# Performance work log

Hardware: AMD Instinct MI355X
Metric: run time of the kernel (lower is better)

## Reference

```python
import math
import jax
import jax.numpy as jnp
import numpy as np

N = 65536      # n_particles(4) * batch(16384)
Z = 2          # z_dim
CTX = 128      # ctx_dim
H = 128        # drift_hidden
TE = 32        # time_emb_dim
T = 51         # n_integration_steps + 1
MAX_FREQ = 10.0


def setup_inputs() -> dict:
    key = jax.random.key(0)
    ks = jax.random.split(key, 18)
    rn = lambda k, shp, s=1.0: (jax.random.normal(k, shp, dtype=jnp.float32) * s)
    d_in = Z + CTX + TE   # 162, drift MLP input
    c_in = Z + CTX + 1    # 131, cnf field MLP input
    return {
        'z0': rn(ks[0], (N, Z)),
        'posterior_ctx': rn(ks[1], (N, CTX)),
        'cnf_ctx': rn(ks[2], (N, CTX)),
        'times': jnp.linspace(0.0, 1.0, T, dtype=jnp.float32),
        'xi': rn(ks[3], (T - 1, N, Z)),  # pre-drawn Euler-Maruyama noise
        'freqs': jnp.exp(jnp.linspace(0.0, math.log(MAX_FREQ), TE // 2)).astype(jnp.float32),
        'log_diff': jnp.float32(-3.0),
        'W1': rn(ks[4], (d_in, H), 1.0 / math.sqrt(d_in)),
        'b1': jnp.zeros((H,), jnp.float32),
        'W2': rn(ks[5], (H, H), 1.0 / math.sqrt(H)),
        'b2': jnp.zeros((H,), jnp.float32),
        'W3': rn(ks[6], (H, Z), 1.0 / math.sqrt(H)),
        'b3': jnp.zeros((Z,), jnp.float32),
        'V1': rn(ks[7], (c_in, H), 1.0 / math.sqrt(c_in)),
        'c1': jnp.zeros((H,), jnp.float32),
        'V2': rn(ks[8], (H, H), 1.0 / math.sqrt(H)),
        'c2': jnp.zeros((H,), jnp.float32),
        'V3': rn(ks[9], (H, Z), 1.0 / math.sqrt(H)),
        'c3': jnp.zeros((Z,), jnp.float32),
    }


def reference(z0, posterior_ctx, cnf_ctx, times, xi, freqs, log_diff,
              W1, b1, W2, b2, W3, b3, V1, c1, V2, c2, V3, c3):
    n = z0.shape[0]
    g_base = jax.nn.softplus(log_diff)  # diffusion_scale = 1.0

    def fourier(t):  # scalar t -> [n, TE]
        args = (2.0 * math.pi) * t * freqs  # [TE//2]
        emb = jnp.concatenate([jnp.sin(args), jnp.cos(args)])  # [TE]
        return jnp.broadcast_to(emb[None, :], (n, TE))

    def post_drift(z, t):  # PosteriorDriftNet: 3-layer MLP on [z, ctx, temb]
        inp = jnp.concatenate([z, posterior_ctx, fourier(t)], axis=-1)  # [n, 162]
        h = jax.nn.relu(inp @ W1 + b1)
        h = jax.nn.relu(h @ W2 + b2)
        return h @ W3 + b3  # [n, Z]

    def cnf_field(z, t):  # stand-in for cnf.eval_field(z, ctx, t); length_scale = 1.0
        tcol = jnp.broadcast_to(jnp.reshape(t, (1, 1)), (n, 1))
        inp = jnp.concatenate([z, cnf_ctx, tcol], axis=-1)  # [n, 131]
        h = jnp.tanh(inp @ V1 + c1)
        h = jnp.tanh(h @ V2 + c2)
        return h @ V3 + c3  # [n, Z]

    def step(z, per_step):  # Euler drift + Euler-Maruyama diffusion
        t_i, t_next, xi_i = per_step
        dt = t_next - t_i
        g = g_base * (1.0 - t_i)  # time_decay ** 1
        drift = cnf_field(z, t_i) + post_drift(z, t_i)
        z_prop = z + drift * dt
        z_new = z_prop + xi_i * (g * jnp.sqrt(jnp.maximum(dt, 1e-12)))
        return z_new, z_new

    _, traj_tail = jax.lax.scan(step, z0, (times[:-1], times[1:], xi))
    traj = jnp.concatenate([z0[None], traj_tail], axis=0)  # [T, n, Z]
    return traj
```

## Files before the change

kernel.cpp:

```cpp
#include <hip/hip_runtime.h>
#include <hip/hip_bf16.h>
#include <math.h>

#define NP 65536
#define HD 128
#define TSTEPS 50

typedef short bf16x8 __attribute__((ext_vector_type(8)));
typedef float f32x4 __attribute__((ext_vector_type(4)));
typedef float f32x2 __attribute__((ext_vector_type(2)));

__device__ __forceinline__ short f2bf(float f) {
    union { float f; unsigned u; } v; v.f = f;
    unsigned r = v.u + 0x7fffu + ((v.u >> 16) & 1u);
    return (short)(r >> 16);
}
__device__ __forceinline__ unsigned cvt_pk_bf16(float a, float b) {
    __hip_bfloat162 h = __float22bfloat162_rn(make_float2(a, b));
    unsigned u;
    __builtin_memcpy(&u, &h, sizeof(u));
    return u;
}

__device__ __forceinline__ f32x2 pk_fma(f32x2 a, f32x2 b, f32x2 c) {
    return __builtin_elementwise_fma(a, b, c);
}
__device__ __forceinline__ f32x2 pk_add(f32x2 a, f32x2 b) { return a + b; }
__device__ __forceinline__ f32x2 pk_mul(f32x2 a, f32x2 b) { return a * b; }

__device__ __forceinline__ f32x2 tanh_pk(f32x2 x, f32x2 k2, f32x2 one2, f32x2 m2) {
    f32x2 t = pk_mul(x, k2);
    f32x2 e;
    e.x = __builtin_amdgcn_exp2f(t.x);
    e.y = __builtin_amdgcn_exp2f(t.y);
    f32x2 dn = pk_add(e, one2);
    f32x2 r;
    r.x = __builtin_amdgcn_rcpf(dn.x);
    r.y = __builtin_amdgcn_rcpf(dn.y);
    return pk_fma(r, m2, one2);
}
__device__ __forceinline__ f32x2 shfl_xor_f2(f32x2 v, int off) {
    f32x2 d;
    d.x = __shfl_xor(v.x, off);
    d.y = __shfl_xor(v.y, off);
    return d;
}

__global__ __launch_bounds__(128) void prep_kernel(
    const float* __restrict__ times, const float* __restrict__ freqs,
    const float* __restrict__ log_diff,
    const float* __restrict__ W1, const float* __restrict__ b1,
    const float* __restrict__ V1, const float* __restrict__ c1,
    float* __restrict__ tembW, float* __restrict__ tV,
    float* __restrict__ dtv, float* __restrict__ nsv)
{
    int j = threadIdx.x;
    int i = blockIdx.x;
    float ld = log_diff[0];
    float gb = (ld > 20.0f) ? ld : log1pf(expf(ld));
    float t  = times[i];
    float dt = times[i + 1] - t;
    float acc = b1[j];
    #pragma unroll
    for (int m = 0; m < 16; ++m) {
        float a = 6.283185307179586f * t * freqs[m];
        float sn, cs;
        sincosf(a, &sn, &cs);
        acc = fmaf(sn, W1[(130 + m) * HD + j], acc);
        acc = fmaf(cs, W1[(146 + m) * HD + j], acc);
    }
    tembW[i * HD + j] = acc;
    tV[i * HD + j] = fmaf(t, V1[130 * HD + j], c1[j]);
    if (j == 0) {
        dtv[i] = dt;
        nsv[i] = gb * (1.0f - t) * sqrtf(fmaxf(dt, 1e-12f));
    }
}

__global__ __launch_bounds__(256) void pack_kernel(
    const float* __restrict__ W1, const float* __restrict__ V1,
    const float* __restrict__ W2, const float* __restrict__ V2,
    short* __restrict__ packed)
{
    int gi = blockIdx.x * 256 + threadIdx.x;
    int mat = gi >> 14;
    int s = gi & 16383;
    int j  = s & 7;
    int cc = (s >> 3) & 15;
    int qq = (s >> 7) & 3;
    int kt = (s >> 9) & 3;
    int jt = (s >> 11) & 7;
    int k = kt * 32 + qq * 8 + j;
    int n = jt * 16 + cc;
    float v;
    if      (mat == 0) v = W1[(2 + k) * HD + n];
    else if (mat == 1) v = V1[(2 + k) * HD + n];
    else if (mat == 2) v = W2[k * HD + n];
    else               v = V2[k * HD + n];
    packed[gi] = f2bf(v);
}

__global__ __launch_bounds__(256, 2) void sde_kernel(
    const float* __restrict__ z0, const float* __restrict__ pctx,
    const float* __restrict__ cctx, const float* __restrict__ xi,
    const short* __restrict__ packedW,
    const float* __restrict__ W1, const float* __restrict__ V1,
    const float* __restrict__ b2, const float* __restrict__ c2,
    const float* __restrict__ W3, const float* __restrict__ b3,
    const float* __restrict__ V3, const float* __restrict__ c3,
    const float* __restrict__ tembW, const float* __restrict__ tV,
    const float* __restrict__ dtv, const float* __restrict__ nsv,
    float* __restrict__ out)
{
    __shared__ char smem[80896];
    float* stg = (float*)smem;
    const bf16x8* ldsF = (const bf16x8*)smem;
    float*  zwP0s = (float*)(smem + 67584);
    float*  zwP1s = (float*)(smem + 68096);
    float*  zwC0s = (float*)(smem + 68608);
    float*  zwC1s = (float*)(smem + 69120);
    float*  b2s   = (float*)(smem + 69632);
    float*  c2s   = (float*)(smem + 70144);
    float2* w3s   = (float2*)(smem + 70656);
    float2* v3s   = (float2*)(smem + 71680);

    int tid = threadIdx.x;
    int lane = tid & 63, wv = tid >> 6;
    int q = lane >> 4, c = lane & 15;
    int m0 = blockIdx.x * 64 + wv * 16;
    int mrow = m0 + c;

    float* tslot = (float*)(smem + 72704) + wv * 512;

    if (tid < 128) {
        zwP0s[tid] = W1[tid];
        zwP1s[tid] = W1[HD + tid];
        zwC0s[tid] = V1[tid];
        zwC1s[tid] = V1[HD + tid];
        b2s[tid] = b2[tid];
        c2s[tid] = c2[tid];
        w3s[tid] = ((const float2*)W3)[tid];
        v3s[tid] = ((const float2*)V3)[tid];
    }

    {
        const uint4* src = (const uint4*)packedW;
        uint4* dst = (uint4*)smem;
        #pragma unroll
        for (int i = 0; i < 16; ++i) dst[i * 256 + tid] = src[i * 256 + tid];
    }
    __syncthreads();

    bf16x8 pf[4], cf[4];
    #pragma unroll
    for (int kt = 0; kt < 4; ++kt) {
        const float4* p4 = (const float4*)(pctx + (size_t)mrow * HD + kt * 32 + q * 8);
        float4 a = p4[0], b = p4[1];
        uint4 tu;
        tu.x = cvt_pk_bf16(a.x, a.y); tu.y = cvt_pk_bf16(a.z, a.w);
        tu.z = cvt_pk_bf16(b.x, b.y); tu.w = cvt_pk_bf16(b.z, b.w);
        __builtin_memcpy(&pf[kt], &tu, 16);
        const float4* c4 = (const float4*)(cctx + (size_t)mrow * HD + kt * 32 + q * 8);
        float4 e = c4[0], d = c4[1];
        uint4 uu;
        uu.x = cvt_pk_bf16(e.x, e.y); uu.y = cvt_pk_bf16(e.z, e.w);
        uu.z = cvt_pk_bf16(d.x, d.y); uu.w = cvt_pk_bf16(d.z, d.w);
        __builtin_memcpy(&cf[kt], &uu, 16);
    }

    f32x4 accP[8], accC[8];
    #pragma unroll
    for (int jt = 0; jt < 8; ++jt) {
        f32x4 ap = {0.f,0.f,0.f,0.f}, ac = {0.f,0.f,0.f,0.f};
        #pragma unroll
        for (int kt = 0; kt < 4; ++kt) {
            int fi = ((jt * 4 + kt) * 4 + q) * 16 + c;
            ap = __builtin_amdgcn_mfma_f32_16x16x32_bf16(pf[kt], ldsF[fi], ap, 0, 0, 0);
            ac = __builtin_amdgcn_mfma_f32_16x16x32_bf16(cf[kt], ldsF[2048 + fi], ac, 0, 0, 0);
        }
        accP[jt] = ap; accC[jt] = ac;
    }
    __syncthreads();

    #pragma unroll
    for (int jt = 0; jt < 8; ++jt)
        #pragma unroll
        for (int r = 0; r < 4; ++r) {
            stg[(wv * 16 + q * 4 + r) * 132 + jt * 16 + c]        = accP[jt][r];
            stg[8448 + (wv * 16 + q * 4 + r) * 132 + jt * 16 + c] = accC[jt][r];
        }
    __syncthreads();
    f32x2 projPf[16], projCf[16];
    #pragma unroll
    for (int kt = 0; kt < 4; ++kt) {
        const float4* rp = (const float4*)(stg + (wv * 16 + c) * 132 + kt * 32 + q * 8);
        float4 a = rp[0], b = rp[1];
        projPf[kt*4+0] = (f32x2){a.x, a.y}; projPf[kt*4+1] = (f32x2){a.z, a.w};
        projPf[kt*4+2] = (f32x2){b.x, b.y}; projPf[kt*4+3] = (f32x2){b.z, b.w};
        const float4* rc = (const float4*)(stg + 8448 + (wv * 16 + c) * 132 + kt * 32 + q * 8);
        float4 e = rc[0], d = rc[1];
        projCf[kt*4+0] = (f32x2){e.x, e.y}; projCf[kt*4+1] = (f32x2){e.z, e.w};
        projCf[kt*4+2] = (f32x2){d.x, d.y}; projCf[kt*4+3] = (f32x2){d.z, d.w};
    }
    __syncthreads();

    {
        const uint4* src = (const uint4*)(packedW + 32768);
        uint4* dst = (uint4*)smem;
        #pragma unroll
        for (int i = 0; i < 16; ++i) dst[i * 256 + tid] = src[i * 256 + tid];
    }
    __syncthreads();

    float b3x = b3[0] + c3[0], b3y = b3[1] + c3[1];
    const f32x2 k2   = {2.8853900817779268f, 2.8853900817779268f};
    const f32x2 one2 = {1.0f, 1.0f};
    const f32x2 m2   = {-2.0f, -2.0f};

    const float2* z02 = (const float2*)z0;
    const float2* xi2 = (const float2*)xi;
    float2* out2 = (float2*)out;

    {
        const float4* srcp = (lane < 32)
            ? ((const float4*)(tV) + lane)
            : ((const float4*)(tembW) + (lane - 32));
        *((float4*)tslot + lane) = *srcp;
    }

    float2 zi = z02[mrow];
    float zx = zi.x, zy = zi.y;
    int row_mine = q * 4 + (c & 3);
    if (lane < 16) out2[m0 + lane] = make_float2(zx, zy);

    for (int i = 0; i < TSTEPS; ++i) {
        int b = i & 1;
        const float* tb = tslot + b * 256;

        int sN = (i + 1 < TSTEPS) ? i + 1 : i;
        float4 pfv;
        {
            const float4* srcp = (lane < 32)
                ? ((const float4*)(tV + sN * HD) + lane)
                : ((const float4*)(tembW + sN * HD) + (lane - 32));
            pfv = *srcp;
        }
        float dt = dtv[i], ns = nsv[i];
        float2 xiv = xi2[(size_t)i * NP + m0 + row_mine];

        f32x2 zx2 = {zx, zx}, zy2 = {zy, zy};
        f32x2 px01 = {b3x, b3x}, px23 = px01;
        f32x2 py01 = {b3y, b3y}, py23 = py01;

        bf16x8 af[4];
        #pragma unroll
        for (int kt = 0; kt < 4; ++kt) {
            const f32x2* tvp = (const f32x2*)(tb + kt * 32 + q * 8);
            const f32x2* w0p = (const f32x2*)(zwC0s + kt * 32 + q * 8);
            const f32x2* w1p = (const f32x2*)(zwC1s + kt * 32 + q * 8);
            uint4 tu;
            unsigned uu[4];
            #pragma unroll
            for (int p = 0; p < 4; ++p) {
                f32x2 lin = pk_add(projCf[kt * 4 + p], tvp[p]);
                lin = pk_fma(zx2, w0p[p], lin);
                lin = pk_fma(zy2, w1p[p], lin);
                f32x2 th = tanh_pk(lin, k2, one2, m2);
                uu[p] = cvt_pk_bf16(th.x, th.y);
            }
            tu.x = uu[0]; tu.y = uu[1]; tu.z = uu[2]; tu.w = uu[3];
            __builtin_memcpy(&af[kt], &tu, 16);
        }
        #pragma unroll
        for (int jt = 0; jt < 8; ++jt) {
            float cb = c2s[jt * 16 + c];
            f32x4 acc = {cb, cb, cb, cb};
            #pragma unroll
            for (int kt = 0; kt < 4; ++kt)
                acc = __builtin_amdgcn_mfma_f32_16x16x32_bf16(
                    af[kt], ldsF[2048 + ((jt * 4 + kt) * 4 + q) * 16 + c], acc, 0, 0, 0);
            f32x2 a01 = {acc[0], acc[1]};
            f32x2 a23 = {acc[2], acc[3]};
            f32x2 h01 = tanh_pk(a01, k2, one2, m2);
            f32x2 h23 = tanh_pk(a23, k2, one2, m2);
            float2 v3 = v3s[jt * 16 + c];
            f32x2 v3x = {v3.x, v3.x}, v3y = {v3.y, v3.y};
            px01 = pk_fma(h01, v3x, px01); px23 = pk_fma(h23, v3x, px23);
            py01 = pk_fma(h01, v3y, py01); py23 = pk_fma(h23, v3y, py23);
        }

        #pragma unroll
        for (int kt = 0; kt < 4; ++kt) {
            const f32x2* tvp = (const f32x2*)(tb + 128 + kt * 32 + q * 8);
            const f32x2* w0p = (const f32x2*)(zwP0s + kt * 32 + q * 8);
            const f32x2* w1p = (const f32x2*)(zwP1s + kt * 32 + q * 8);
            uint4 tu;
            unsigned uu[4];
            #pragma unroll
            for (int p = 0; p < 4; ++p) {
                f32x2 lin = pk_add(projPf[kt * 4 + p], tvp[p]);
                lin = pk_fma(zx2, w0p[p], lin);
                lin = pk_fma(zy2, w1p[p], lin);
                f32x2 th;
                th.x = fmaxf(lin.x, 0.0f);
                th.y = fmaxf(lin.y, 0.0f);
                uu[p] = cvt_pk_bf16(th.x, th.y);
            }
            tu.x = uu[0]; tu.y = uu[1]; tu.z = uu[2]; tu.w = uu[3];
            __builtin_memcpy(&af[kt], &tu, 16);
        }
        #pragma unroll
        for (int jt = 0; jt < 8; ++jt) {
            float bb = b2s[jt * 16 + c];
            f32x4 acc = {bb, bb, bb, bb};
            #pragma unroll
            for (int kt = 0; kt < 4; ++kt)
                acc = __builtin_amdgcn_mfma_f32_16x16x32_bf16(
                    af[kt], ldsF[((jt * 4 + kt) * 4 + q) * 16 + c], acc, 0, 0, 0);
            f32x2 h01, h23;
            h01.x = fmaxf(acc[0], 0.0f); h01.y = fmaxf(acc[1], 0.0f);
            h23.x = fmaxf(acc[2], 0.0f); h23.y = fmaxf(acc[3], 0.0f);
            float2 w3 = w3s[jt * 16 + c];
            f32x2 w3x = {w3.x, w3.x}, w3y = {w3.y, w3.y};
            px01 = pk_fma(h01, w3x, px01); px23 = pk_fma(h23, w3x, px23);
            py01 = pk_fma(h01, w3y, py01); py23 = pk_fma(h23, w3y, py23);
        }

        *((float4*)(tslot + (b ^ 1) * 256) + lane) = pfv;

        #pragma unroll
        for (int off = 1; off < 16; off <<= 1) {
            px01 = pk_add(px01, shfl_xor_f2(px01, off));
            px23 = pk_add(px23, shfl_xor_f2(px23, off));
            py01 = pk_add(py01, shfl_xor_f2(py01, off));
            py23 = pk_add(py23, shfl_xor_f2(py23, off));
        }

        int cc = c & 3;
        float sdx = px01.x, sdy = py01.x;
        sdx = (cc == 1) ? px01.y : sdx; sdy = (cc == 1) ? py01.y : sdy;
        sdx = (cc == 2) ? px23.x : sdx; sdy = (cc == 2) ? py23.x : sdy;
        sdx = (cc == 3) ? px23.y : sdx; sdy = (cc == 3) ? py23.y : sdy;
        float zox = __shfl(zx, row_mine), zoy = __shfl(zy, row_mine);
        float znx = fmaf(sdx, dt, zox) + xiv.x * ns;
        float zny = fmaf(sdy, dt, zoy) + xiv.y * ns;

        int src_store = ((lane >> 2) << 4) | (lane & 3);
        float sx = __shfl(znx, src_store);
        float sy = __shfl(zny, src_store);
        if (lane < 16) out2[(size_t)(i + 1) * NP + m0 + lane] = make_float2(sx, sy);

        int src_z = ((c >> 2) << 4) | (c & 3);
        zx = __shfl(znx, src_z);
        zy = __shfl(zny, src_z);
    }
}

extern "C" void kernel_launch(void* const* d_in, const int* in_sizes, int n_in,
                              void* d_out, int out_size, void* d_ws, size_t ws_size,
                              hipStream_t stream)
{
    const float* z0    = (const float*)d_in[0];
    const float* pctx  = (const float*)d_in[1];
    const float* cctx  = (const float*)d_in[2];
    const float* times = (const float*)d_in[3];
    const float* xi    = (const float*)d_in[4];
    const float* freqs = (const float*)d_in[5];
    const float* logd  = (const float*)d_in[6];
    const float* W1 = (const float*)d_in[7];
    const float* b1 = (const float*)d_in[8];
    const float* W2 = (const float*)d_in[9];
    const float* b2 = (const float*)d_in[10];
    const float* W3 = (const float*)d_in[11];
    const float* b3 = (const float*)d_in[12];
    const float* V1 = (const float*)d_in[13];
    const float* c1 = (const float*)d_in[14];
    const float* V2 = (const float*)d_in[15];
    const float* c2 = (const float*)d_in[16];
    const float* V3 = (const float*)d_in[17];
    const float* c3 = (const float*)d_in[18];

    short* packedW = (short*)d_ws;
    float* tembW = (float*)((char*)d_ws + 131072);
    float* tV    = tembW + TSTEPS * HD;
    float* dtv   = tV + TSTEPS * HD;
    float* nsv   = dtv + 64;

    prep_kernel<<<TSTEPS, 128, 0, stream>>>(times, freqs, logd, W1, b1, V1, c1,
                                            tembW, tV, dtv, nsv);
    pack_kernel<<<256, 256, 0, stream>>>(W1, V1, W2, V2, packedW);
    sde_kernel<<<NP / 64, 256, 0, stream>>>(z0, pctx, cctx, xi, packedW,
                                            W1, V1, b2, c2, W3, b3, V3, c3,
                                            tembW, tV, dtv, nsv,
                                            (float*)d_out);
}
```

Measured before the change: 637.9 us.

## Process two 16-row tiles per wave to reuse weight fragments and add ILP

Each wave now handles 32 particles (two 16-row MFMA tiles A and B) instead of 16, and the grid is halved to NP/128 blocks. Every weight fragment read from LDS now feeds two MFMAs, and the two independent chains give the scheduler more instruction-level parallelism to hide MFMA and tanh latency. The cost is roughly double the register footprint (projections, accumulators and activations for both tiles), which may lower occupancy or cause spills, and there are fewer blocks to spread across the CUs.

```diff
diff --git a/kernel.cpp b/kernel.cpp
--- a/kernel.cpp
+++ b/kernel.cpp
@@ -127,8 +127,9 @@
     int tid = threadIdx.x;
     int lane = tid & 63, wv = tid >> 6;
     int q = lane >> 4, c = lane & 15;
-    int m0 = blockIdx.x * 64 + wv * 16;
-    int mrow = m0 + c;
+    int m0 = blockIdx.x * 128 + wv * 32;
+    int mrowA = m0 + c;
+    int mrowB = m0 + 16 + c;
 
     float* tslot = (float*)(smem + 72704) + wv * 512;
 
@@ -151,56 +152,96 @@
     }
     __syncthreads();
 
-    bf16x8 pf[4], cf[4];
+    bf16x8 pfA[4], cfA[4], pfB[4], cfB[4];
     #pragma unroll
     for (int kt = 0; kt < 4; ++kt) {
-        const float4* p4 = (const float4*)(pctx + (size_t)mrow * HD + kt * 32 + q * 8);
-        float4 a = p4[0], b = p4[1];
-        uint4 tu;
-        tu.x = cvt_pk_bf16(a.x, a.y); tu.y = cvt_pk_bf16(a.z, a.w);
-        tu.z = cvt_pk_bf16(b.x, b.y); tu.w = cvt_pk_bf16(b.z, b.w);
-        __builtin_memcpy(&pf[kt], &tu, 16);
-        const float4* c4 = (const float4*)(cctx + (size_t)mrow * HD + kt * 32 + q * 8);
-        float4 e = c4[0], d = c4[1];
-        uint4 uu;
-        uu.x = cvt_pk_bf16(e.x, e.y); uu.y = cvt_pk_bf16(e.z, e.w);
-        uu.z = cvt_pk_bf16(d.x, d.y); uu.w = cvt_pk_bf16(d.z, d.w);
-        __builtin_memcpy(&cf[kt], &uu, 16);
-    }
-
-    f32x4 accP[8], accC[8];
+        {
+            const float4* p4 = (const float4*)(pctx + (size_t)mrowA * HD + kt * 32 + q * 8);
+            float4 a = p4[0], b = p4[1];
+            uint4 tu;
+            tu.x = cvt_pk_bf16(a.x, a.y); tu.y = cvt_pk_bf16(a.z, a.w);
+            tu.z = cvt_pk_bf16(b.x, b.y); tu.w = cvt_pk_bf16(b.z, b.w);
+            __builtin_memcpy(&pfA[kt], &tu, 16);
+            const float4* c4 = (const float4*)(cctx + (size_t)mrowA * HD + kt * 32 + q * 8);
+            float4 e = c4[0], d = c4[1];
+            uint4 uu;
+            uu.x = cvt_pk_bf16(e.x, e.y); uu.y = cvt_pk_bf16(e.z, e.w);
+            uu.z = cvt_pk_bf16(d.x, d.y); uu.w = cvt_pk_bf16(d.z, d.w);
+            __builtin_memcpy(&cfA[kt], &uu, 16);
+        }
+        {
+            const float4* p4 = (const float4*)(pctx + (size_t)mrowB * HD + kt * 32 + q * 8);
+            float4 a = p4[0], b = p4[1];
+            uint4 tu;
+            tu.x = cvt_pk_bf16(a.x, a.y); tu.y = cvt_pk_bf16(a.z, a.w);
+            tu.z = cvt_pk_bf16(b.x, b.y); tu.w = cvt_pk_bf16(b.z, b.w);
+            __builtin_memcpy(&pfB[kt], &tu, 16);
+            const float4* c4 = (const float4*)(cctx + (size_t)mrowB * HD + kt * 32 + q * 8);
+            float4 e = c4[0], d = c4[1];
+            uint4 uu;
+            uu.x = cvt_pk_bf16(e.x, e.y); uu.y = cvt_pk_bf16(e.z, e.w);
+            uu.z = cvt_pk_bf16(d.x, d.y); uu.w = cvt_pk_bf16(d.z, d.w);
+            __builtin_memcpy(&cfB[kt], &uu, 16);
+        }
+    }
+
+    f32x4 accPA[8], accCA[8], accPB[8], accCB[8];
     #pragma unroll
     for (int jt = 0; jt < 8; ++jt) {
-        f32x4 ap = {0.f,0.f,0.f,0.f}, ac = {0.f,0.f,0.f,0.f};
+        f32x4 apA = {0.f,0.f,0.f,0.f}, acA = apA, apB = apA, acB = apA;
         #pragma unroll
         for (int kt = 0; kt < 4; ++kt) {
             int fi = ((jt * 4 + kt) * 4 + q) * 16 + c;
-            ap = __builtin_amdgcn_mfma_f32_16x16x32_bf16(pf[kt], ldsF[fi], ap, 0, 0, 0);
-            ac = __builtin_amdgcn_mfma_f32_16x16x32_bf16(cf[kt], ldsF[2048 + fi], ac, 0, 0, 0);
-        }
-        accP[jt] = ap; accC[jt] = ac;
-    }
-    __syncthreads();
-
+            bf16x8 wP = ldsF[fi];
+            bf16x8 wC = ldsF[2048 + fi];
+            apA = __builtin_amdgcn_mfma_f32_16x16x32_bf16(pfA[kt], wP, apA, 0, 0, 0);
+            apB = __builtin_amdgcn_mfma_f32_16x16x32_bf16(pfB[kt], wP, apB, 0, 0, 0);
+            acA = __builtin_amdgcn_mfma_f32_16x16x32_bf16(cfA[kt], wC, acA, 0, 0, 0);
+            acB = __builtin_amdgcn_mfma_f32_16x16x32_bf16(cfB[kt], wC, acB, 0, 0, 0);
+        }
+        accPA[jt] = apA; accCA[jt] = acA; accPB[jt] = apB; accCB[jt] = acB;
+    }
+    __syncthreads();
+
+    f32x2 projPfA[16], projCfA[16], projPfB[16], projCfB[16];
     #pragma unroll
     for (int jt = 0; jt < 8; ++jt)
         #pragma unroll
         for (int r = 0; r < 4; ++r) {
-            stg[(wv * 16 + q * 4 + r) * 132 + jt * 16 + c]        = accP[jt][r];
-            stg[8448 + (wv * 16 + q * 4 + r) * 132 + jt * 16 + c] = accC[jt][r];
-        }
-    __syncthreads();
-    f32x2 projPf[16], projCf[16];
+            stg[(wv * 16 + q * 4 + r) * 132 + jt * 16 + c]        = accPA[jt][r];
+            stg[8448 + (wv * 16 + q * 4 + r) * 132 + jt * 16 + c] = accCA[jt][r];
+        }
+    __syncthreads();
     #pragma unroll
     for (int kt = 0; kt < 4; ++kt) {
         const float4* rp = (const float4*)(stg + (wv * 16 + c) * 132 + kt * 32 + q * 8);
         float4 a = rp[0], b = rp[1];
-        projPf[kt*4+0] = (f32x2){a.x, a.y}; projPf[kt*4+1] = (f32x2){a.z, a.w};
-        projPf[kt*4+2] = (f32x2){b.x, b.y}; projPf[kt*4+3] = (f32x2){b.z, b.w};
+        projPfA[kt*4+0] = (f32x2){a.x, a.y}; projPfA[kt*4+1] = (f32x2){a.z, a.w};
+        projPfA[kt*4+2] = (f32x2){b.x, b.y}; projPfA[kt*4+3] = (f32x2){b.z, b.w};
         const float4* rc = (const float4*)(stg + 8448 + (wv * 16 + c) * 132 + kt * 32 + q * 8);
         float4 e = rc[0], d = rc[1];
-        projCf[kt*4+0] = (f32x2){e.x, e.y}; projCf[kt*4+1] = (f32x2){e.z, e.w};
-        projCf[kt*4+2] = (f32x2){d.x, d.y}; projCf[kt*4+3] = (f32x2){d.z, d.w};
+        projCfA[kt*4+0] = (f32x2){e.x, e.y}; projCfA[kt*4+1] = (f32x2){e.z, e.w};
+        projCfA[kt*4+2] = (f32x2){d.x, d.y}; projCfA[kt*4+3] = (f32x2){d.z, d.w};
+    }
+    __syncthreads();
+    #pragma unroll
+    for (int jt = 0; jt < 8; ++jt)
+        #pragma unroll
+        for (int r = 0; r < 4; ++r) {
+            stg[(wv * 16 + q * 4 + r) * 132 + jt * 16 + c]        = accPB[jt][r];
+            stg[8448 + (wv * 16 + q * 4 + r) * 132 + jt * 16 + c] = accCB[jt][r];
+        }
+    __syncthreads();
+    #pragma unroll
+    for (int kt = 0; kt < 4; ++kt) {
+        const float4* rp = (const float4*)(stg + (wv * 16 + c) * 132 + kt * 32 + q * 8);
+        float4 a = rp[0], b = rp[1];
+        projPfB[kt*4+0] = (f32x2){a.x, a.y}; projPfB[kt*4+1] = (f32x2){a.z, a.w};
+        projPfB[kt*4+2] = (f32x2){b.x, b.y}; projPfB[kt*4+3] = (f32x2){b.z, b.w};
+        const float4* rc = (const float4*)(stg + 8448 + (wv * 16 + c) * 132 + kt * 32 + q * 8);
+        float4 e = rc[0], d = rc[1];
+        projCfB[kt*4+0] = (f32x2){e.x, e.y}; projCfB[kt*4+1] = (f32x2){e.z, e.w};
+        projCfB[kt*4+2] = (f32x2){d.x, d.y}; projCfB[kt*4+3] = (f32x2){d.z, d.w};
     }
     __syncthreads();
 
@@ -228,10 +269,14 @@
         *((float4*)tslot + lane) = *srcp;
     }
 
-    float2 zi = z02[mrow];
-    float zx = zi.x, zy = zi.y;
+    float2 ziA = z02[mrowA], ziB = z02[mrowB];
+    float zxA = ziA.x, zyA = ziA.y;
+    float zxB = ziB.x, zyB = ziB.y;
     int row_mine = q * 4 + (c & 3);
-    if (lane < 16) out2[m0 + lane] = make_float2(zx, zy);
+    if (lane < 16) {
+        out2[m0 + lane]      = make_float2(zxA, zyA);
+        out2[m0 + 16 + lane] = make_float2(zxB, zyB);
+    }
 
     for (int i = 0; i < TSTEPS; ++i) {
         int b = i & 1;
@@ -246,47 +291,71 @@
             pfv = *srcp;
         }
         float dt = dtv[i], ns = nsv[i];
-        float2 xiv = xi2[(size_t)i * NP + m0 + row_mine];
-
-        f32x2 zx2 = {zx, zx}, zy2 = {zy, zy};
-        f32x2 px01 = {b3x, b3x}, px23 = px01;
-        f32x2 py01 = {b3y, b3y}, py23 = py01;
-
-        bf16x8 af[4];
+        float2 xivA = xi2[(size_t)i * NP + m0 + row_mine];
+        float2 xivB = xi2[(size_t)i * NP + m0 + 16 + row_mine];
+
+        f32x2 zxA2 = {zxA, zxA}, zyA2 = {zyA, zyA};
+        f32x2 zxB2 = {zxB, zxB}, zyB2 = {zyB, zyB};
+        f32x2 pxA01 = {b3x, b3x}, pxA23 = pxA01;
+        f32x2 pyA01 = {b3y, b3y}, pyA23 = pyA01;
+        f32x2 pxB01 = {b3x, b3x}, pxB23 = pxB01;
+        f32x2 pyB01 = {b3y, b3y}, pyB23 = pyB01;
+
+        bf16x8 afA[4], afB[4];
         #pragma unroll
         for (int kt = 0; kt < 4; ++kt) {
             const f32x2* tvp = (const f32x2*)(tb + kt * 32 + q * 8);
             const f32x2* w0p = (const f32x2*)(zwC0s + kt * 32 + q * 8);
             const f32x2* w1p = (const f32x2*)(zwC1s + kt * 32 + q * 8);
-            uint4 tu;
-            unsigned uu[4];
+            uint4 tuA, tuB;
+            unsigned uuA[4], uuB[4];
             #pragma unroll
             for (int p = 0; p < 4; ++p) {
-                f32x2 lin = pk_add(projCf[kt * 4 + p], tvp[p]);
-                lin = pk_fma(zx2, w0p[p], lin);
-                lin = pk_fma(zy2, w1p[p], lin);
-                f32x2 th = tanh_pk(lin, k2, one2, m2);
-                uu[p] = cvt_pk_bf16(th.x, th.y);
-            }
-            tu.x = uu[0]; tu.y = uu[1]; tu.z = uu[2]; tu.w = uu[3];
-            __builtin_memcpy(&af[kt], &tu, 16);
+                f32x2 tv = tvp[p], w0 = w0p[p], w1 = w1p[p];
+                f32x2 linA = pk_add(projCfA[kt * 4 + p], tv);
+                linA = pk_fma(zxA2, w0, linA);
+                linA = pk_fma(zyA2, w1, linA);
+                f32x2 thA = tanh_pk(linA, k2, one2, m2);
+                uuA[p] = cvt_pk_bf16(thA.x, thA.y);
+                f32x2 linB = pk_add(projCfB[kt * 4 + p], tv);
+                linB = pk_fma(zxB2, w0, linB);
+                linB = pk_fma(zyB2, w1, linB);
+                f32x2 thB = tanh_pk(linB, k2, one2, m2);
+                uuB[p] = cvt_pk_bf16(thB.x, thB.y);
+            }
+            tuA.x = uuA[0]; tuA.y = uuA[1]; tuA.z = uuA[2]; tuA.w = uuA[3];
+            __builtin_memcpy(&afA[kt], &tuA, 16);
+            tuB.x = uuB[0]; tuB.y = uuB[1]; tuB.z = uuB[2]; tuB.w = uuB[3];
+            __builtin_memcpy(&afB[kt], &tuB, 16);
         }
         #pragma unroll
         for (int jt = 0; jt < 8; ++jt) {
             float cb = c2s[jt * 16 + c];
-            f32x4 acc = {cb, cb, cb, cb};
+            f32x4 accA = {cb, cb, cb, cb}, accB = accA;
             #pragma unroll
-            for (int kt = 0; kt < 4; ++kt)
-                acc = __builtin_amdgcn_mfma_f32_16x16x32_bf16(
-                    af[kt], ldsF[2048 + ((jt * 4 + kt) * 4 + q) * 16 + c], acc, 0, 0, 0);
-            f32x2 a01 = {acc[0], acc[1]};
-            f32x2 a23 = {acc[2], acc[3]};
-            f32x2 h01 = tanh_pk(a01, k2, one2, m2);
-            f32x2 h23 = tanh_pk(a23, k2, one2, m2);
+            for (int kt = 0; kt < 4; ++kt) {
+                bf16x8 bw = ldsF[2048 + ((jt * 4 + kt) * 4 + q) * 16 + c];
+                accA = __builtin_amdgcn_mfma_f32_16x16x32_bf16(afA[kt], bw, accA, 0, 0, 0);
+                accB = __builtin_amdgcn_mfma_f32_16x16x32_bf16(afB[kt], bw, accB, 0, 0, 0);
+            }
             float2 v3 = v3s[jt * 16 + c];
             f32x2 v3x = {v3.x, v3.x}, v3y = {v3.y, v3.y};
-            px01 = pk_fma(h01, v3x, px01); px23 = pk_fma(h23, v3x, px23);
-            py01 = pk_fma(h01, v3y, py01); py23 = pk_fma(h23, v3y, py23);
+            {
+                f32x2 a01 = {accA[0], accA[1]};
+                f32x2 a23 = {accA[2], accA[3]};
+                f32x2 h01 = tanh_pk(a01, k2, one2, m2);
+                f32x2 h23 = tanh_pk(a23, k2, one2, m2);
+                pxA01 = pk_fma(h01, v3x, pxA01); pxA23 = pk_fma(h23, v3x, pxA23);
+                pyA01 = pk_fma(h01, v3y, pyA01); pyA23 = pk_fma(h23, v3y, pyA23);
+            }
+            {
+                f32x2 a01 = {accB[0], accB[1]};
+                f32x2 a23 = {accB[2], accB[3]};
+                f32x2 h01 = tanh_pk(a01, k2, one2, m2);
+                f32x2 h23 = tanh_pk(a23, k2, one2, m2);
+                pxB01 = pk_fma(h01, v3x, pxB01); pxB23 = pk_fma(h23, v3x, pxB23);
+                pyB01 = pk_fma(h01, v3y, pyB01); pyB23 = pk_fma(h23, v3y, pyB23);
+            }
         }
 
         #pragma unroll
@@ -294,65 +363,98 @@
             const f32x2* tvp = (const f32x2*)(tb + 128 + kt * 32 + q * 8);
             const f32x2* w0p = (const f32x2*)(zwP0s + kt * 32 + q * 8);
             const f32x2* w1p = (const f32x2*)(zwP1s + kt * 32 + q * 8);
-            uint4 tu;
-            unsigned uu[4];
+            uint4 tuA, tuB;
+            unsigned uuA[4], uuB[4];
             #pragma unroll
             for (int p = 0; p < 4; ++p) {
-                f32x2 lin = pk_add(projPf[kt * 4 + p], tvp[p]);
-                lin = pk_fma(zx2, w0p[p], lin);
-                lin = pk_fma(zy2, w1p[p], lin);
-                f32x2 th;
-                th.x = fmaxf(lin.x, 0.0f);
-                th.y = fmaxf(lin.y, 0.0f);
-                uu[p] = cvt_pk_bf16(th.x, th.y);
-            }
-            tu.x = uu[0]; tu.y = uu[1]; tu.z = uu[2]; tu.w = uu[3];
-            __builtin_memcpy(&af[kt], &tu, 16);
+                f32x2 tv = tvp[p], w0 = w0p[p], w1 = w1p[p];
+                f32x2 linA = pk_add(projPfA[kt * 4 + p], tv);
+                linA = pk_fma(zxA2, w0, linA);
+                linA = pk_fma(zyA2, w1, linA);
+                uuA[p] = cvt_pk_bf16(fmaxf(linA.x, 0.0f), fmaxf(linA.y, 0.0f));
+                f32x2 linB = pk_add(projPfB[kt * 4 + p], tv);
+                linB = pk_fma(zxB2, w0, linB);
+                linB = pk_fma(zyB2, w1, linB);
+                uuB[p] = cvt_pk_bf16(fmaxf(linB.x, 0.0f), fmaxf(linB.y, 0.0f));
+            }
+            tuA.x = uuA[0]; tuA.y = uuA[1]; tuA.z = uuA[2]; tuA.w = uuA[3];
+            __builtin_memcpy(&afA[kt], &tuA, 16);
+            tuB.x = uuB[0]; tuB.y = uuB[1]; tuB.z = uuB[2]; tuB.w = uuB[3];
+            __builtin_memcpy(&afB[kt], &tuB, 16);
         }
         #pragma unroll
         for (int jt = 0; jt < 8; ++jt) {
             float bb = b2s[jt * 16 + c];
-            f32x4 acc = {bb, bb, bb, bb};
+            f32x4 accA = {bb, bb, bb, bb}, accB = accA;
             #pragma unroll
-            for (int kt = 0; kt < 4; ++kt)
-                acc = __builtin_amdgcn_mfma_f32_16x16x32_bf16(
-                    af[kt], ldsF[((jt * 4 + kt) * 4 + q) * 16 + c], acc, 0, 0, 0);
-            f32x2 h01, h23;
-            h01.x = fmaxf(acc[0], 0.0f); h01.y = fmaxf(acc[1], 0.0f);
-            h23.x = fmaxf(acc[2], 0.0f); h23.y = fmaxf(acc[3], 0.0f);
+            for (int kt = 0; kt < 4; ++kt) {
+                bf16x8 bw = ldsF[((jt * 4 + kt) * 4 + q) * 16 + c];
+                accA = __builtin_amdgcn_mfma_f32_16x16x32_bf16(afA[kt], bw, accA, 0, 0, 0);
+                accB = __builtin_amdgcn_mfma_f32_16x16x32_bf16(afB[kt], bw, accB, 0, 0, 0);
+            }
             float2 w3 = w3s[jt * 16 + c];
             f32x2 w3x = {w3.x, w3.x}, w3y = {w3.y, w3.y};
-            px01 = pk_fma(h01, w3x, px01); px23 = pk_fma(h23, w3x, px23);
-            py01 = pk_fma(h01, w3y, py01); py23 = pk_fma(h23, w3y, py23);
+            {
+                f32x2 h01, h23;
+                h01.x = fmaxf(accA[0], 0.0f); h01.y = fmaxf(accA[1], 0.0f);
+                h23.x = fmaxf(accA[2], 0.0f); h23.y = fmaxf(accA[3], 0.0f);
+                pxA01 = pk_fma(h01, w3x, pxA01); pxA23 = pk_fma(h23, w3x, pxA23);
+                pyA01 = pk_fma(h01, w3y, pyA01); pyA23 = pk_fma(h23, w3y, pyA23);
+            }
+            {
+                f32x2 h01, h23;
+                h01.x = fmaxf(accB[0], 0.0f); h01.y = fmaxf(accB[1], 0.0f);
+                h23.x = fmaxf(accB[2], 0.0f); h23.y = fmaxf(accB[3], 0.0f);
+                pxB01 = pk_fma(h01, w3x, pxB01); pxB23 = pk_fma(h23, w3x, pxB23);
+                pyB01 = pk_fma(h01, w3y, pyB01); pyB23 = pk_fma(h23, w3y, pyB23);
+            }
         }
 
         *((float4*)(tslot + (b ^ 1) * 256) + lane) = pfv;
 
         #pragma unroll
         for (int off = 1; off < 16; off <<= 1) {
-            px01 = pk_add(px01, shfl_xor_f2(px01, off));
-            px23 = pk_add(px23, shfl_xor_f2(px23, off));
-            py01 = pk_add(py01, shfl_xor_f2(py01, off));
-            py23 = pk_add(py23, shfl_xor_f2(py23, off));
+            pxA01 = pk_add(pxA01, shfl_xor_f2(pxA01, off));
+            pxB01 = pk_add(pxB01, shfl_xor_f2(pxB01, off));
+            pxA23 = pk_add(pxA23, shfl_xor_f2(pxA23, off));
+            pxB23 = pk_add(pxB23, shfl_xor_f2(pxB23, off));
+            pyA01 = pk_add(pyA01, shfl_xor_f2(pyA01, off));
+            pyB01 = pk_add(pyB01, shfl_xor_f2(pyB01, off));
+            pyA23 = pk_add(pyA23, shfl_xor_f2(pyA23, off));
+            pyB23 = pk_add(pyB23, shfl_xor_f2(pyB23, off));
         }
 
         int cc = c & 3;
-        float sdx = px01.x, sdy = py01.x;
-        sdx = (cc == 1) ? px01.y : sdx; sdy = (cc == 1) ? py01.y : sdy;
-        sdx = (cc == 2) ? px23.x : sdx; sdy = (cc == 2) ? py23.x : sdy;
-        sdx = (cc == 3) ? px23.y : sdx; sdy = (cc == 3) ? py23.y : sdy;
-        float zox = __shfl(zx, row_mine), zoy = __shfl(zy, row_mine);
-        float znx = fmaf(sdx, dt, zox) + xiv.x * ns;
-        float zny = fmaf(sdy, dt, zoy) + xiv.y * ns;
-
-        int src_store = ((lane >> 2) << 4) | (lane & 3);
-        float sx = __shfl(znx, src_store);
-        float sy = __shfl(zny, src_store);
-        if (lane < 16) out2[(size_t)(i + 1) * NP + m0 + lane] = make_float2(sx, sy);
+        float sdxA = pxA01.x, sdyA = pyA01.x;
+        sdxA = (cc == 1) ? pxA01.y : sdxA; sdyA = (cc == 1) ? pyA01.y : sdyA;
+        sdxA = (cc == 2) ? pxA23.x : sdxA; sdyA = (cc == 2) ? pyA23.x : sdyA;
+        sdxA = (cc == 3) ? pxA23.y : sdxA; sdyA = (cc == 3) ? pyA23.y : sdyA;
+        float sdxB = pxB01.x, sdyB = pyB01.x;
+        sdxB = (cc == 1) ? pxB01.y : sdxB; sdyB = (cc == 1) ? pyB01.y : sdyB;
+        sdxB = (cc == 2) ? pxB23.x : sdxB; sdyB = (cc == 2) ? pyB23.x : sdyB;
+        sdxB = (cc == 3) ? pxB23.y : sdxB; sdyB = (cc == 3) ? pyB23.y : sdyB;
+        float zoxA = __shfl(zxA, row_mine), zoyA = __shfl(zyA, row_mine);
+        float zoxB = __shfl(zxB, row_mine), zoyB = __shfl(zyB, row_mine);
+        float znxA = fmaf(sdxA, dt, zoxA) + xivA.x * ns;
+        float znyA = fmaf(sdyA, dt, zoyA) + xivA.y * ns;
+        float znxB = fmaf(sdxB, dt, zoxB) + xivB.x * ns;
+        float znyB = fmaf(sdyB, dt, zoyB) + xivB.y * ns;
+
+        int ls = lane & 15;
+        int src_store = ((ls >> 2) << 4) | (ls & 3);
+        float sxA = __shfl(znxA, src_store), syA = __shfl(znyA, src_store);
+        float sxB = __shfl(znxB, src_store), syB = __shfl(znyB, src_store);
+        if (lane < 32) {
+            float sx = (lane < 16) ? sxA : sxB;
+            float sy = (lane < 16) ? syA : syB;
+            out2[(size_t)(i + 1) * NP + m0 + lane] = make_float2(sx, sy);
+        }
 
         int src_z = ((c >> 2) << 4) | (c & 3);
-        zx = __shfl(znx, src_z);
-        zy = __shfl(zny, src_z);
+        zxA = __shfl(znxA, src_z);
+        zyA = __shfl(znyA, src_z);
+        zxB = __shfl(znxB, src_z);
+        zyB = __shfl(znyB, src_z);
     }
 }
 
@@ -389,8 +491,8 @@
     prep_kernel<<<TSTEPS, 128, 0, stream>>>(times, freqs, logd, W1, b1, V1, c1,
                                             tembW, tV, dtv, nsv);
     pack_kernel<<<256, 256, 0, stream>>>(W1, V1, W2, V2, packedW);
-    sde_kernel<<<NP / 64, 256, 0, stream>>>(z0, pctx, cctx, xi, packedW,
-                                            W1, V1, b2, c2, W3, b3, V3, c3,
-                                            tembW, tV, dtv, nsv,
-                                            (float*)d_out);
-}
+    sde_kernel<<<NP / 128, 256, 0, stream>>>(z0, pctx, cctx, xi, packedW,
+                                             W1, V1, b2, c2, W3, b3, V3, c3,
+                                             tembW, tV, dtv, nsv,
+                                             (float*)d_out);
+}
```

Result: slower. 658.5 us (+3.2%).

## Swap MFMA operands to put rows in lanes and shrink drift reduction

Applied to the files above, without the earlier changes.

Swaps the A/B operands of the layer-2 MFMAs so each lane's accumulator holds four hidden units for its own particle row rather than four rows for one hidden unit. The output projection then accumulates into a single packed pair per lane, and the cross-lane reduction shrinks from four xor-shuffle rounds over four vectors to two rounds over scalars. This removes the per-step row-select and the redistribution shuffles of z. Biases and W3/V3 are now read as vectors per lane-group, and ReLU uses a packed max.

```diff
diff --git a/kernel.cpp b/kernel.cpp
--- a/kernel.cpp
+++ b/kernel.cpp
@@ -27,6 +27,9 @@
 }
 __device__ __forceinline__ f32x2 pk_add(f32x2 a, f32x2 b) { return a + b; }
 __device__ __forceinline__ f32x2 pk_mul(f32x2 a, f32x2 b) { return a * b; }
+__device__ __forceinline__ f32x2 pk_max(f32x2 a, f32x2 b) {
+    return __builtin_elementwise_max(a, b);
+}
 
 __device__ __forceinline__ f32x2 tanh_pk(f32x2 x, f32x2 k2, f32x2 one2, f32x2 m2) {
     f32x2 t = pk_mul(x, k2);
@@ -38,12 +41,6 @@
     r.x = __builtin_amdgcn_rcpf(dn.x);
     r.y = __builtin_amdgcn_rcpf(dn.y);
     return pk_fma(r, m2, one2);
-}
-__device__ __forceinline__ f32x2 shfl_xor_f2(f32x2 v, int off) {
-    f32x2 d;
-    d.x = __shfl_xor(v.x, off);
-    d.y = __shfl_xor(v.y, off);
-    return d;
 }
 
 __global__ __launch_bounds__(128) void prep_kernel(
@@ -213,9 +210,10 @@
     __syncthreads();
 
     float b3x = b3[0] + c3[0], b3y = b3[1] + c3[1];
-    const f32x2 k2   = {2.8853900817779268f, 2.8853900817779268f};
-    const f32x2 one2 = {1.0f, 1.0f};
-    const f32x2 m2   = {-2.0f, -2.0f};
+    const f32x2 k2    = {2.8853900817779268f, 2.8853900817779268f};
+    const f32x2 one2  = {1.0f, 1.0f};
+    const f32x2 m2    = {-2.0f, -2.0f};
+    const f32x2 zero2 = {0.0f, 0.0f};
 
     const float2* z02 = (const float2*)z0;
     const float2* xi2 = (const float2*)xi;
@@ -230,7 +228,6 @@
 
     float2 zi = z02[mrow];
     float zx = zi.x, zy = zi.y;
-    int row_mine = q * 4 + (c & 3);
     if (lane < 16) out2[m0 + lane] = make_float2(zx, zy);
 
     for (int i = 0; i < TSTEPS; ++i) {
@@ -246,11 +243,10 @@
             pfv = *srcp;
         }
         float dt = dtv[i], ns = nsv[i];
-        float2 xiv = xi2[(size_t)i * NP + m0 + row_mine];
+        float2 xiv = xi2[(size_t)i * NP + m0 + c];
 
         f32x2 zx2 = {zx, zx}, zy2 = {zy, zy};
-        f32x2 px01 = {b3x, b3x}, px23 = px01;
-        f32x2 py01 = {b3y, b3y}, py23 = py01;
+        f32x2 px2 = zero2, py2 = zero2;
 
         bf16x8 af[4];
         #pragma unroll
@@ -273,20 +269,20 @@
         }
         #pragma unroll
         for (int jt = 0; jt < 8; ++jt) {
-            float cb = c2s[jt * 16 + c];
-            f32x4 acc = {cb, cb, cb, cb};
+            const float4 cb4 = *(const float4*)(c2s + jt * 16 + q * 4);
+            f32x4 acc = {cb4.x, cb4.y, cb4.z, cb4.w};
             #pragma unroll
             for (int kt = 0; kt < 4; ++kt)
                 acc = __builtin_amdgcn_mfma_f32_16x16x32_bf16(
-                    af[kt], ldsF[2048 + ((jt * 4 + kt) * 4 + q) * 16 + c], acc, 0, 0, 0);
-            f32x2 a01 = {acc[0], acc[1]};
-            f32x2 a23 = {acc[2], acc[3]};
-            f32x2 h01 = tanh_pk(a01, k2, one2, m2);
-            f32x2 h23 = tanh_pk(a23, k2, one2, m2);
-            float2 v3 = v3s[jt * 16 + c];
-            f32x2 v3x = {v3.x, v3.x}, v3y = {v3.y, v3.y};
-            px01 = pk_fma(h01, v3x, px01); px23 = pk_fma(h23, v3x, px23);
-            py01 = pk_fma(h01, v3y, py01); py23 = pk_fma(h23, v3y, py23);
+                    ldsF[2048 + ((jt * 4 + kt) * 4 + q) * 16 + c], af[kt], acc, 0, 0, 0);
+            f32x2 h01 = tanh_pk((f32x2){acc[0], acc[1]}, k2, one2, m2);
+            f32x2 h23 = tanh_pk((f32x2){acc[2], acc[3]}, k2, one2, m2);
+            const float2* vp = v3s + jt * 16 + q * 4;
+            float2 v0 = vp[0], v1 = vp[1], v2 = vp[2], v3v = vp[3];
+            f32x2 vx01 = {v0.x, v1.x}, vx23 = {v2.x, v3v.x};
+            f32x2 vy01 = {v0.y, v1.y}, vy23 = {v2.y, v3v.y};
+            px2 = pk_fma(h01, vx01, px2); px2 = pk_fma(h23, vx23, px2);
+            py2 = pk_fma(h01, vy01, py2); py2 = pk_fma(h23, vy23, py2);
         }
 
         #pragma unroll
@@ -301,9 +297,7 @@
                 f32x2 lin = pk_add(projPf[kt * 4 + p], tvp[p]);
                 lin = pk_fma(zx2, w0p[p], lin);
                 lin = pk_fma(zy2, w1p[p], lin);
-                f32x2 th;
-                th.x = fmaxf(lin.x, 0.0f);
-                th.y = fmaxf(lin.y, 0.0f);
+                f32x2 th = pk_max(lin, zero2);
                 uu[p] = cvt_pk_bf16(th.x, th.y);
             }
             tu.x = uu[0]; tu.y = uu[1]; tu.z = uu[2]; tu.w = uu[3];
@@ -311,48 +305,36 @@
         }
         #pragma unroll
         for (int jt = 0; jt < 8; ++jt) {
-            float bb = b2s[jt * 16 + c];
-            f32x4 acc = {bb, bb, bb, bb};
+            const float4 bb4 = *(const float4*)(b2s + jt * 16 + q * 4);
+            f32x4 acc = {bb4.x, bb4.y, bb4.z, bb4.w};
             #pragma unroll
             for (int kt = 0; kt < 4; ++kt)
                 acc = __builtin_amdgcn_mfma_f32_16x16x32_bf16(
-                    af[kt], ldsF[((jt * 4 + kt) * 4 + q) * 16 + c], acc, 0, 0, 0);
-            f32x2 h01, h23;
-            h01.x = fmaxf(acc[0], 0.0f); h01.y = fmaxf(acc[1], 0.0f);
-            h23.x = fmaxf(acc[2], 0.0f); h23.y = fmaxf(acc[3], 0.0f);
-            float2 w3 = w3s[jt * 16 + c];
-            f32x2 w3x = {w3.x, w3.x}, w3y = {w3.y, w3.y};
-            px01 = pk_fma(h01, w3x, px01); px23 = pk_fma(h23, w3x, px23);
-            py01 = pk_fma(h01, w3y, py01); py23 = pk_fma(h23, w3y, py23);
+                    ldsF[((jt * 4 + kt) * 4 + q) * 16 + c], af[kt], acc, 0, 0, 0);
+            f32x2 h01 = pk_max((f32x2){acc[0], acc[1]}, zero2);
+            f32x2 h23 = pk_max((f32x2){acc[2], acc[3]}, zero2);
+            const float2* wp = w3s + jt * 16 + q * 4;
+            float2 w0 = wp[0], w1 = wp[1], w2 = wp[2], w3v = wp[3];
+            f32x2 wx01 = {w0.x, w1.x}, wx23 = {w2.x, w3v.x};
+            f32x2 wy01 = {w0.y, w1.y}, wy23 = {w2.y, w3v.y};
+            px2 = pk_fma(h01, wx01, px2); px2 = pk_fma(h23, wx23, px2);
+            py2 = pk_fma(h01, wy01, py2); py2 = pk_fma(h23, wy23, py2);
         }
 
         *((float4*)(tslot + (b ^ 1) * 256) + lane) = pfv;
 
-        #pragma unroll
-        for (int off = 1; off < 16; off <<= 1) {
-            px01 = pk_add(px01, shfl_xor_f2(px01, off));
-            px23 = pk_add(px23, shfl_xor_f2(px23, off));
-            py01 = pk_add(py01, shfl_xor_f2(py01, off));
-            py23 = pk_add(py23, shfl_xor_f2(py23, off));
-        }
-
-        int cc = c & 3;
-        float sdx = px01.x, sdy = py01.x;
-        sdx = (cc == 1) ? px01.y : sdx; sdy = (cc == 1) ? py01.y : sdy;
-        sdx = (cc == 2) ? px23.x : sdx; sdy = (cc == 2) ? py23.x : sdy;
-        sdx = (cc == 3) ? px23.y : sdx; sdy = (cc == 3) ? py23.y : sdy;
-        float zox = __shfl(zx, row_mine), zoy = __shfl(zy, row_mine);
-        float znx = fmaf(sdx, dt, zox) + xiv.x * ns;
-        float zny = fmaf(sdy, dt, zoy) + xiv.y * ns;
-
-        int src_store = ((lane >> 2) << 4) | (lane & 3);
-        float sx = __shfl(znx, src_store);
-        float sy = __shfl(zny, src_store);
-        if (lane < 16) out2[(size_t)(i + 1) * NP + m0 + lane] = make_float2(sx, sy);
-
-        int src_z = ((c >> 2) << 4) | (c & 3);
-        zx = __shfl(znx, src_z);
-        zy = __shfl(zny, src_z);
+        float sdx = px2.x + px2.y + b3x;
+        float sdy = py2.x + py2.y + b3y;
+        sdx += __shfl_xor(sdx, 16);
+        sdy += __shfl_xor(sdy, 16);
+        sdx += __shfl_xor(sdx, 32);
+        sdy += __shfl_xor(sdy, 32);
+
+        float znx = fmaf(sdx, dt, zx) + xiv.x * ns;
+        float zny = fmaf(sdy, dt, zy) + xiv.y * ns;
+        if (lane < 16) out2[(size_t)(i + 1) * NP + m0 + lane] = make_float2(znx, zny);
+        zx = znx;
+        zy = zny;
     }
 }
 
```

Result: no change. 629.4 us (-1.3%).
